# Kernel optimization log

Hardware: AMD Instinct MI355X
Metric: run time of the kernel (lower is better)

Reference implementation:

```python
import jax, jax.numpy as jnp
import numpy as np

NQ = 4
PI_HALF = np.pi / 2
HAD = jnp.array([[1, 1], [1, -1]], dtype=jnp.complex64) / np.sqrt(2)
CNOT = jnp.array([[1, 0, 0, 0], [0, 1, 0, 0], [0, 0, 0, 1], [0, 0, 1, 0]], dtype=jnp.complex64)
_bits = (np.arange(2 ** NQ)[:, None] >> np.arange(NQ - 1, -1, -1)[None, :]) & 1
ZSIGNS = jnp.asarray(1.0 - 2.0 * _bits, jnp.float32)  # [16, NQ]


def _ry(theta):
    c = jnp.cos(theta / 2).astype(jnp.complex64)
    s = jnp.sin(theta / 2).astype(jnp.complex64)
    return jnp.stack([jnp.stack([c, -s], -1), jnp.stack([s, c], -1)], -2)  # [...,2,2]


def _rot(phi, theta, omega):
    # PennyLane Rot = RZ(omega) @ RY(theta) @ RZ(phi)
    c = jnp.cos(theta / 2).astype(jnp.complex64)
    s = jnp.sin(theta / 2).astype(jnp.complex64)
    ep = jnp.exp(0.5j * phi).astype(jnp.complex64)
    eo = jnp.exp(0.5j * omega).astype(jnp.complex64)
    return jnp.stack([jnp.stack([jnp.conj(ep) * jnp.conj(eo) * c, -ep * jnp.conj(eo) * s]),
                      jnp.stack([jnp.conj(ep) * eo * s, ep * eo * c])])


def _cry(theta):
    # controlled-RY, batched: [B] -> [B,4,4], basis order (control, target)
    B = theta.shape[0]
    U = jnp.zeros((B, 4, 4), jnp.complex64).at[:, 0, 0].set(1.0).at[:, 1, 1].set(1.0)
    return U.at[:, 2:, 2:].set(_ry(theta))


def _apply1(state, U, wire):
    s = jnp.moveaxis(state, wire + 1, 1)
    shp = s.shape
    s = s.reshape(shp[0], 2, -1)
    s = jnp.einsum('ij,bjk->bik', U, s) if U.ndim == 2 else jnp.einsum('bij,bjk->bik', U, s)
    return jnp.moveaxis(s.reshape(shp), 1, wire + 1)


def _apply2(state, U, q0, q1):
    s = jnp.moveaxis(state, (q0 + 1, q1 + 1), (1, 2))
    shp = s.shape
    s = s.reshape(shp[0], 4, -1)
    s = jnp.einsum('ij,bjk->bik', U, s) if U.ndim == 2 else jnp.einsum('bij,bjk->bik', U, s)
    return jnp.moveaxis(s.reshape(shp), (1, 2), (q0 + 1, q1 + 1))


def _init_state(B):
    s = jnp.zeros((B, 2 ** NQ), jnp.complex64).at[:, 0].set(1.0)
    return s.reshape((B,) + (2,) * NQ)


def _zexp(state):
    p = state.reshape(state.shape[0], -1)
    p = p.real ** 2 + p.imag ** 2
    return p @ ZSIGNS  # [B, NQ]


def _attention_circuit(q, k, params):
    # q, k: [E, NQ] angles; params: [NQ, 3] shared
    s = _init_state(q.shape[0])
    for i in range(NQ):
        s = _apply1(s, _ry(q[:, i]), i)
    for i in range(NQ):
        s = _apply1(s, HAD, i)
    for i in range(NQ):
        s = _apply2(s, _cry(k[:, i]), i, (i + 1) % NQ)
    for i in range(NQ):
        s = _apply1(s, _rot(params[i, 0], params[i, 1], params[i, 2]), i)
    return _zexp(s)


def _entangle_circuit(x, params):
    # x: [N, NQ] angles; params: [n_layers, NQ, 3]
    s = _init_state(x.shape[0])
    for i in range(NQ):
        s = _apply1(s, _ry(x[:, i]), i)
    for l in range(params.shape[0]):
        for i in range(NQ - 1):
            s = _apply2(s, CNOT, i, i + 1)
        for i in range(NQ):
            s = _apply1(s, _rot(params[l, i, 0], params[l, i, 1], params[l, i, 2]), i)
        s = _apply2(s, CNOT, 0, NQ - 1)  # n_qubits >= 4
    return _zexp(s)


def _path_circuit(x, params):
    # x: [N, NQ]; params: [3, NQ, 3]
    s = _init_state(x.shape[0])
    for i in range(NQ):
        s = _apply1(s, HAD, i)
    for i in range(NQ):
        s = _apply1(s, _ry(x[:, i]), i)
    for l in range(3):
        for i in range(NQ):
            s = _apply1(s, _rot(params[l, i, 0], params[l, i, 1], params[l, i, 2]), i)
        for i in range(NQ - 1):
            s = _apply2(s, CNOT, i, i + 1)
    return _zexp(s)


def _forward(x, W_in, b_in, lin_W, lin_b, qproj_W, qproj_b, ent_params,
             attq_W, attq_b, attk_W, attk_b, att_qp, path_params,
             path_in_W, path_in_b, path_out_W, path_out_b, out_W, out_b, edge_index):
    N = x.shape[0]
    loops = jnp.arange(N, dtype=edge_index.dtype)
    ei = jnp.concatenate([edge_index, jnp.stack([loops, loops])], axis=1)  # add_self_loops
    src, dst = ei[0], ei[1]
    h = jax.nn.relu(x @ W_in.T + b_in)
    for l in range(lin_W.shape[0]):
        x_cls = h @ lin_W[l].T + lin_b[l]
        xq = _entangle_circuit(jnp.tanh(h[:, :NQ]) * PI_HALF, ent_params[l])
        x_comb = x_cls + xq @ qproj_W[l].T + qproj_b[l]
        q = jnp.tanh(h @ attq_W[l].T + attq_b[l]) * PI_HALF
        k = jnp.tanh(h @ attk_W[l].T + attk_b[l]) * PI_HALF
        scores = _attention_circuit(q[src], k[dst], att_qp[l]).mean(axis=1)  # [E]
        att = jax.nn.softmax(scores)  # global softmax over all edges (faithful)
        h = jax.ops.segment_sum(att[:, None] * x_comb[src], dst, num_segments=N)
        h = jax.nn.relu(h)  # dropout is identity at eval
    pq = jnp.tanh(h @ path_in_W.T + path_in_b) * PI_HALF
    h = _path_circuit(pq, path_params) @ path_out_W.T + path_out_b
    return h @ out_W.T + out_b


def setup_inputs() -> dict:
    key = jax.random.key(0)
    ks = jax.random.split(key, 22)
    N, E, D_in, D_h, D_out, L = 20000, 300000, 64, 128, 32, 2
    w = lambda k, shape: jax.random.normal(k, shape, jnp.float32) * 0.1
    return {
        'x': jax.random.normal(ks[0], (N, D_in), jnp.float32),
        'W_in': w(ks[1], (D_h, D_in)), 'b_in': w(ks[2], (D_h,)),
        'lin_W': w(ks[3], (L, D_h, D_h)), 'lin_b': w(ks[4], (L, D_h)),
        'qproj_W': w(ks[5], (L, D_h, NQ)), 'qproj_b': w(ks[6], (L, D_h)),
        'ent_params': w(ks[7], (L, 2, NQ, 3)),
        'attq_W': w(ks[8], (L, NQ, D_h)), 'attq_b': w(ks[9], (L, NQ)),
        'attk_W': w(ks[10], (L, NQ, D_h)), 'attk_b': w(ks[11], (L, NQ)),
        'att_qp': w(ks[12], (L, NQ, 3)),
        'path_params': w(ks[13], (3, NQ, 3)),
        'path_in_W': w(ks[14], (NQ, D_h)), 'path_in_b': w(ks[15], (NQ,)),
        'path_out_W': w(ks[16], (D_h, NQ)), 'path_out_b': w(ks[17], (D_h,)),
        'out_W': w(ks[18], (D_out, D_h)), 'out_b': w(ks[19], (D_out,)),
        'edge_index': jax.random.randint(ks[20], (2, E), 0, N, dtype=jnp.int32),
    }


def reference(x, W_in, b_in, lin_W, lin_b, qproj_W, qproj_b, ent_params,
              attq_W, attq_b, attk_W, attk_b, att_qp, path_params,
              path_in_W, path_in_b, path_out_W, path_out_b, out_W, out_b, edge_index):
    return _forward(x, W_in, b_in, lin_W, lin_b, qproj_W, qproj_b, ent_params,
                    attq_W, attq_b, attk_W, attk_b, att_qp, path_params,
                    path_in_W, path_in_b, path_out_W, path_out_b, out_W, out_b, edge_index)
```

## Files before the change

### kernel.cpp

```cpp
#include <hip/hip_runtime.h>
#include <math.h>

#define PI_HALF 1.57079632679489662f

__device__ __forceinline__ float fast_tanh(float x) {
    float e = __expf(2.f * x);
    return 1.f - 2.f * __builtin_amdgcn_rcpf(e + 1.f);
}


__device__ __forceinline__ void init_state(float sr[16], float si[16]) {
#pragma unroll
    for (int i = 0; i < 16; ++i) { sr[i] = 0.f; si[i] = 0.f; }
    sr[0] = 1.f;
}

template<int M>
__device__ __forceinline__ void ry_g(float sr[16], float si[16], float c, float s) {
#pragma unroll
    for (int i = 0; i < 16; ++i) {
        if (i & M) continue;
        const int j = i | M;
        float ar = sr[i], ai = si[i], br = sr[j], bi = si[j];
        sr[i] = c * ar - s * br;  si[i] = c * ai - s * bi;
        sr[j] = s * ar + c * br;  si[j] = s * ai + c * bi;
    }
}

template<int M>
__device__ __forceinline__ void had_g(float sr[16], float si[16]) {
    const float r = 0.70710678118654752f;
#pragma unroll
    for (int i = 0; i < 16; ++i) {
        if (i & M) continue;
        const int j = i | M;
        float ar = sr[i], ai = si[i], br = sr[j], bi = si[j];
        sr[i] = (ar + br) * r;  si[i] = (ai + bi) * r;
        sr[j] = (ar - br) * r;  si[j] = (ai - bi) * r;
    }
}

template<int MC, int MT>
__device__ __forceinline__ void cnot_g(float sr[16], float si[16]) {
#pragma unroll
    for (int i = 0; i < 16; ++i) {
        if (!(i & MC) || (i & MT)) continue;
        const int j = i | MT;
        float tr = sr[i], ti = si[i];
        sr[i] = sr[j]; si[i] = si[j];
        sr[j] = tr;    si[j] = ti;
    }
}

template<int MC, int MT>
__device__ __forceinline__ void cry_g(float sr[16], float si[16], float c, float s) {
#pragma unroll
    for (int i = 0; i < 16; ++i) {
        if (!(i & MC) || (i & MT)) continue;
        const int j = i | MT;
        float ar = sr[i], ai = si[i], br = sr[j], bi = si[j];
        sr[i] = c * ar - s * br;  si[i] = c * ai - s * bi;
        sr[j] = s * ar + c * br;  si[j] = s * ai + c * bi;
    }
}

template<int M>
__device__ __forceinline__ void rot_pre(float sr[16], float si[16], const float* __restrict__ u) {
    const float u00r = u[0], u00i = u[1], u01r = u[2], u01i = u[3];
    const float u10r = u[4], u10i = u[5], u11r = u[6], u11i = u[7];
#pragma unroll
    for (int i = 0; i < 16; ++i) {
        if (i & M) continue;
        const int j = i | M;
        float ar = sr[i], ai = si[i], br = sr[j], bi = si[j];
        sr[i] = u00r * ar - u00i * ai + u01r * br - u01i * bi;
        si[i] = u00r * ai + u00i * ar + u01r * bi + u01i * br;
        sr[j] = u10r * ar - u10i * ai + u11r * br - u11i * bi;
        si[j] = u10r * ai + u10i * ar + u11r * bi + u11i * br;
    }
}

__device__ __forceinline__ void zexp_g(const float sr[16], const float si[16], float z[4]) {
    float p[16];
#pragma unroll
    for (int i = 0; i < 16; ++i) p[i] = sr[i] * sr[i] + si[i] * si[i];
    z[0] = z[1] = z[2] = z[3] = 0.f;
#pragma unroll
    for (int i = 0; i < 16; ++i) {
        z[0] += (i & 8) ? -p[i] : p[i];
        z[1] += (i & 4) ? -p[i] : p[i];
        z[2] += (i & 2) ? -p[i] : p[i];
        z[3] += (i & 1) ? -p[i] : p[i];
    }
}

__global__ void k_setup(const float* __restrict__ entp, const float* __restrict__ attqp,
                        const float* __restrict__ pparm,
                        const float* __restrict__ outW, const float* __restrict__ outb,
                        const float* __restrict__ poW, const float* __restrict__ pob,
                        float* __restrict__ rotbuf, float* __restrict__ M,
                        float* __restrict__ v) {
    const int t = threadIdx.x;
    if (t < 36) {
        const float* p;
        if (t < 16)      p = entp  + t * 3;
        else if (t < 24) p = attqp + (t - 16) * 3;
        else             p = pparm + (t - 24) * 3;
        float phi = p[0], theta = p[1], omega = p[2];
        float st, ct; sincosf(0.5f * theta, &st, &ct);
        float sp, cp; sincosf(0.5f * (phi + omega), &sp, &cp);
        float sm, cm; sincosf(0.5f * (phi - omega), &sm, &cm);
        float* u = rotbuf + t * 8;
        u[0] =  ct * cp;  u[1] = -ct * sp;
        u[2] = -st * cm;  u[3] = -st * sm;
        u[4] =  st * cm;  u[5] = -st * sm;
        u[6] =  ct * cp;  u[7] =  ct * sp;
    } else if (t >= 64 && t < 192) {
        int t2 = t - 64;
        int o = t2 >> 2, i = t2 & 3;
        float acc = 0.f;
        for (int j = 0; j < 128; ++j) acc += outW[o * 128 + j] * poW[j * 4 + i];
        M[t2] = acc;
    } else if (t >= 192 && t < 224) {
        int o = t - 192;
        float acc = outb[o];
        for (int j = 0; j < 128; ++j) acc += outW[o * 128 + j] * pob[j];
        v[o] = acc;
    }
}


__global__ void k_hist(const int* __restrict__ ei, int* __restrict__ cnt, int E, int EP) {
    int e = blockIdx.x * blockDim.x + threadIdx.x;
    if (e >= EP) return;
    int d_ = (e < E) ? ei[E + e] : e - E;
    atomicAdd(&cnt[d_], 1);
}

__global__ void k_scan(const int* __restrict__ cnt, int* __restrict__ off,
                       int* __restrict__ cur, int N) {
    __shared__ int tot[1024];
    const int t = threadIdx.x;
    const int chunk = (N + 1023) >> 10;
    const int s0 = t * chunk;
    const int s1 = min(s0 + chunk, N);
    int sum = 0;
    for (int i = s0; i < s1; ++i) sum += cnt[i];
    tot[t] = sum;
    __syncthreads();
    for (int d = 1; d < 1024; d <<= 1) {
        int v = (t >= d) ? tot[t - d] : 0;
        __syncthreads();
        tot[t] += v;
        __syncthreads();
    }
    int run = (t == 0) ? 0 : tot[t - 1];
    for (int i = s0; i < s1; ++i) {
        off[i] = run; cur[i] = run;
        run += cnt[i];
    }
}

__global__ void k_fill(const int* __restrict__ ei, int* __restrict__ cur,
                       int* __restrict__ srcs, int* __restrict__ dsts, int E, int EP) {
    int e = blockIdx.x * blockDim.x + threadIdx.x;
    if (e >= EP) return;
    int s_, d_;
    if (e < E) { s_ = ei[e]; d_ = ei[E + e]; } else { s_ = d_ = e - E; }
    int pos = atomicAdd(&cur[d_], 1);
    srcs[pos] = s_;
    dsts[pos] = d_;
}


#define XS 68
__global__ __launch_bounds__(256) void k_in(
        const float* __restrict__ x, const float* __restrict__ W,
        const float* __restrict__ b, float* __restrict__ h, int N) {
    __shared__ float xs[16 * XS];
    const int base = blockIdx.x * 16;
    const int tid = threadIdx.x;
    for (int idx = tid; idx < 16 * 64; idx += 256) {
        int n = base + (idx >> 6);
        xs[(idx >> 6) * XS + (idx & 63)] = (n < N) ? x[(size_t)n * 64 + (idx & 63)] : 0.f;
    }
    __syncthreads();
    const int o  = tid & 127;
    const int nh = tid >> 7;
    float acc[8];
#pragma unroll
    for (int i = 0; i < 8; ++i) acc[i] = 0.f;
    const float4* w4 = (const float4*)(W + o * 64);
    for (int c4 = 0; c4 < 16; ++c4) {
        float4 w = w4[c4];
#pragma unroll
        for (int i = 0; i < 8; ++i) {
            float4 hv = *(const float4*)&xs[(nh * 8 + i) * XS + c4 * 4];
            acc[i] += w.x * hv.x + w.y * hv.y + w.z * hv.z + w.w * hv.w;
        }
    }
    const float bb = b[o];
#pragma unroll
    for (int i = 0; i < 8; ++i) {
        int node = base + nh * 8 + i;
        if (node < N) h[(size_t)node * 128 + o] = fmaxf(acc[i] + bb, 0.f);
    }
}

#define HS 132
__global__ __launch_bounds__(256) void k_lin(
        const float* __restrict__ h,
        const float* __restrict__ linW, const float* __restrict__ linb,
        const float* __restrict__ qpW, const float* __restrict__ qpb,
        const float* __restrict__ aqW, const float* __restrict__ aqb,
        const float* __restrict__ akW, const float* __restrict__ akb,
        const float* __restrict__ rotE,
        float* __restrict__ xcomb, float* __restrict__ qbuf,
        float* __restrict__ kbuf, int N) {
    __shared__ float hs[16 * HS];
    __shared__ float zS[16 * 4];
    const int base = blockIdx.x * 16;
    const int tid = threadIdx.x;
    for (int idx = tid; idx < 16 * 128; idx += 256) {
        int n = base + (idx >> 7);
        hs[(idx >> 7) * HS + (idx & 127)] = (n < N) ? h[(size_t)n * 128 + (idx & 127)] : 0.f;
    }
    __syncthreads();

    const int o  = tid & 127;
    const int nh = tid >> 7;
    float acc[8];
#pragma unroll
    for (int i = 0; i < 8; ++i) acc[i] = 0.f;
    const float4* w4 = (const float4*)(linW + o * 128);
    for (int c4 = 0; c4 < 32; ++c4) {
        float4 w = w4[c4];
#pragma unroll
        for (int i = 0; i < 8; ++i) {
            float4 hv = *(const float4*)&hs[(nh * 8 + i) * HS + c4 * 4];
            acc[i] += w.x * hv.x + w.y * hv.y + w.z * hv.z + w.w * hv.w;
        }
    }

    if (tid < 128) {
        const int nl = tid >> 3;
        const int which = tid & 7;
        const int qi = which & 3;
        const float4* Wp4 = (const float4*)(((which < 4) ? aqW : akW) + qi * 128);
        float dot = (which < 4) ? aqb[qi] : akb[qi];
        for (int c4 = 0; c4 < 32; ++c4) {
            float4 w = Wp4[c4];
            float4 hv = *(const float4*)&hs[nl * HS + c4 * 4];
            dot += w.x * hv.x + w.y * hv.y + w.z * hv.z + w.w * hv.w;
        }
        int node = base + nl;
        if (node < N) {
            float half = fast_tanh(dot) * (0.5f * PI_HALF);
            float s, c; __sincosf(half, &s, &c);
            float* dst = ((which < 4) ? qbuf : kbuf) + (size_t)node * 8 + qi * 2;
            dst[0] = c; dst[1] = s;
        }
    } else if (tid < 144) {
        const int en = tid - 128;
        float4 hv = *(const float4*)&hs[en * HS];
        float sr[16], si[16];
        init_state(sr, si);
        { float s, c; __sincosf(fast_tanh(hv.x) * (0.5f * PI_HALF), &s, &c); ry_g<8>(sr, si, c, s); }
        { float s, c; __sincosf(fast_tanh(hv.y) * (0.5f * PI_HALF), &s, &c); ry_g<4>(sr, si, c, s); }
        { float s, c; __sincosf(fast_tanh(hv.z) * (0.5f * PI_HALF), &s, &c); ry_g<2>(sr, si, c, s); }
        { float s, c; __sincosf(fast_tanh(hv.w) * (0.5f * PI_HALF), &s, &c); ry_g<1>(sr, si, c, s); }
#pragma unroll
        for (int l = 0; l < 2; ++l) {
            cnot_g<8, 4>(sr, si); cnot_g<4, 2>(sr, si); cnot_g<2, 1>(sr, si);
            const float* P = rotE + l * 32;
            rot_pre<8>(sr, si, P);
            rot_pre<4>(sr, si, P + 8);
            rot_pre<2>(sr, si, P + 16);
            rot_pre<1>(sr, si, P + 24);
            cnot_g<8, 1>(sr, si);
        }
        float z[4]; zexp_g(sr, si, z);
        zS[en * 4 + 0] = z[0]; zS[en * 4 + 1] = z[1];
        zS[en * 4 + 2] = z[2]; zS[en * 4 + 3] = z[3];
    }
    __syncthreads();

    const float bb = linb[o] + qpb[o];
    const float4 qw = *(const float4*)(qpW + o * 4);
#pragma unroll
    for (int i = 0; i < 8; ++i) {
        int node = base + nh * 8 + i;
        if (node < N) {
            float4 z = *(const float4*)&zS[(nh * 8 + i) * 4];
            xcomb[(size_t)node * 128 + o] = acc[i] + bb
                + qw.x * z.x + qw.y * z.y + qw.z * z.z + qw.w * z.w;
        }
    }
}

__global__ void k_att(const float* __restrict__ qb, const float* __restrict__ kb,
                      const int* __restrict__ srcs, const int* __restrict__ dsts,
                      const float* __restrict__ RA, float* __restrict__ escore,
                      float* __restrict__ sumexp, int EP) {
    __shared__ float red[4];
    int p = blockIdx.x * blockDim.x + threadIdx.x;
    float ex = 0.f;
    if (p < EP) {
        int s_ = srcs[p], d_ = dsts[p];
        float4 qa = *(const float4*)&qb[(size_t)s_ * 8];
        float4 qc = *(const float4*)&qb[(size_t)s_ * 8 + 4];
        float4 ka = *(const float4*)&kb[(size_t)d_ * 8];
        float4 kc = *(const float4*)&kb[(size_t)d_ * 8 + 4];
        float sr[16], si[16];
        init_state(sr, si);
        ry_g<8>(sr, si, qa.x, qa.y);
        ry_g<4>(sr, si, qa.z, qa.w);
        ry_g<2>(sr, si, qc.x, qc.y);
        ry_g<1>(sr, si, qc.z, qc.w);
        had_g<8>(sr, si); had_g<4>(sr, si); had_g<2>(sr, si); had_g<1>(sr, si);
        cry_g<8, 4>(sr, si, ka.x, ka.y);
        cry_g<4, 2>(sr, si, ka.z, ka.w);
        cry_g<2, 1>(sr, si, kc.x, kc.y);
        cry_g<1, 8>(sr, si, kc.z, kc.w);
        rot_pre<8>(sr, si, RA);
        rot_pre<4>(sr, si, RA + 8);
        rot_pre<2>(sr, si, RA + 16);
        rot_pre<1>(sr, si, RA + 24);
        float z[4]; zexp_g(sr, si, z);
        float sc = 0.25f * (z[0] + z[1] + z[2] + z[3]);
        ex = __expf(sc);
        escore[p] = ex;
    }
    float w = ex;
#pragma unroll
    for (int d = 32; d > 0; d >>= 1) w += __shfl_down(w, d, 64);
    if ((threadIdx.x & 63) == 0) red[threadIdx.x >> 6] = w;
    __syncthreads();
    if (threadIdx.x == 0)
        atomicAdd(sumexp, red[0] + red[1] + red[2] + red[3]);
}

__global__ void k_gather(const float* __restrict__ xcomb, const int* __restrict__ srcs,
                         const float* __restrict__ escore, const int* __restrict__ off,
                         const int* __restrict__ cnt, const float* __restrict__ sumexp,
                         float* __restrict__ h) {
    __shared__ int sS[128];
    __shared__ float wS[128];
    const int b = blockIdx.x;
    const int tid = threadIdx.x;
    const int start = off[b];
    const int num = cnt[b];
    float acc = 0.f;
    for (int base = 0; base < num; base += 128) {
        int m = min(128, num - base);
        if (tid < m) {
            sS[tid] = srcs[start + base + tid];
            wS[tid] = escore[start + base + tid];
        }
        __syncthreads();
        for (int i = 0; i < m; ++i)
            acc += wS[i] * xcomb[(size_t)sS[i] * 128 + tid];
        __syncthreads();
    }
    const float invS = __builtin_amdgcn_rcpf(sumexp[0]);
    h[(size_t)b * 128 + tid] = fmaxf(acc * invS, 0.f);
}

__global__ __launch_bounds__(256) void k_path(
        const float* __restrict__ h, const float* __restrict__ piW,
        const float* __restrict__ pib, const float* __restrict__ RP,
        const float* __restrict__ M, const float* __restrict__ v,
        float* __restrict__ out, int N) {
    __shared__ float hs[64 * HS];
    __shared__ float pqS[64 * 9];
    __shared__ float zS[64 * 4];
    __shared__ float MS[128];
    __shared__ float vS[32];
    const int base = blockIdx.x * 64;
    const int tid = threadIdx.x;
    if (tid < 128) MS[tid] = M[tid];
    else if (tid < 160) vS[tid - 128] = v[tid - 128];
    for (int idx = tid; idx < 64 * 128; idx += 256) {
        int n = base + (idx >> 7);
        hs[(idx >> 7) * HS + (idx & 127)] = (n < N) ? h[(size_t)n * 128 + (idx & 127)] : 0.f;
    }
    __syncthreads();
    {
        const int nl = tid >> 2;
        const int i  = tid & 3;
        float dot = pib[i];
        const float4* w4 = (const float4*)(piW + i * 128);
        for (int c4 = 0; c4 < 32; ++c4) {
            float4 w = w4[c4];
            float4 hv = *(const float4*)&hs[nl * HS + c4 * 4];
            dot += w.x * hv.x + w.y * hv.y + w.z * hv.z + w.w * hv.w;
        }
        float half = fast_tanh(dot) * (0.5f * PI_HALF);
        float s, c; __sincosf(half, &s, &c);
        pqS[nl * 9 + i * 2]     = c;
        pqS[nl * 9 + i * 2 + 1] = s;
    }
    __syncthreads();
    if (tid < 64) {
        const float* p = pqS + tid * 9;
        float sr[16], si[16];
        init_state(sr, si);
        had_g<8>(sr, si); had_g<4>(sr, si); had_g<2>(sr, si); had_g<1>(sr, si);
        ry_g<8>(sr, si, p[0], p[1]);
        ry_g<4>(sr, si, p[2], p[3]);
        ry_g<2>(sr, si, p[4], p[5]);
        ry_g<1>(sr, si, p[6], p[7]);
#pragma unroll
        for (int l = 0; l < 3; ++l) {
            const float* P = RP + l * 32;
            rot_pre<8>(sr, si, P);
            rot_pre<4>(sr, si, P + 8);
            rot_pre<2>(sr, si, P + 16);
            rot_pre<1>(sr, si, P + 24);
            cnot_g<8, 4>(sr, si); cnot_g<4, 2>(sr, si); cnot_g<2, 1>(sr, si);
        }
        float z[4]; zexp_g(sr, si, z);
        zS[tid * 4 + 0] = z[0]; zS[tid * 4 + 1] = z[1];
        zS[tid * 4 + 2] = z[2]; zS[tid * 4 + 3] = z[3];
    }
    __syncthreads();
#pragma unroll
    for (int k = 0; k < 8; ++k) {
        int flat = k * 256 + tid;
        int nl = flat >> 5;
        int o = flat & 31;
        int node = base + nl;
        if (node < N) {
            out[(size_t)node * 32 + o] = vS[o]
                + MS[o * 4 + 0] * zS[nl * 4 + 0] + MS[o * 4 + 1] * zS[nl * 4 + 1]
                + MS[o * 4 + 2] * zS[nl * 4 + 2] + MS[o * 4 + 3] * zS[nl * 4 + 3];
        }
    }
}


extern "C" void kernel_launch(void* const* d_in, const int* in_sizes, int n_in,
                              void* d_out, int out_size, void* d_ws, size_t ws_size,
                              hipStream_t stream) {
    const float* x     = (const float*)d_in[0];
    const float* W_in  = (const float*)d_in[1];
    const float* b_in  = (const float*)d_in[2];
    const float* linW  = (const float*)d_in[3];
    const float* linb  = (const float*)d_in[4];
    const float* qpW   = (const float*)d_in[5];
    const float* qpb   = (const float*)d_in[6];
    const float* entp  = (const float*)d_in[7];
    const float* aqW   = (const float*)d_in[8];
    const float* aqb   = (const float*)d_in[9];
    const float* akW   = (const float*)d_in[10];
    const float* akb   = (const float*)d_in[11];
    const float* attqp = (const float*)d_in[12];
    const float* pparm = (const float*)d_in[13];
    const float* piW   = (const float*)d_in[14];
    const float* pib   = (const float*)d_in[15];
    const float* poW   = (const float*)d_in[16];
    const float* pob   = (const float*)d_in[17];
    const float* outW  = (const float*)d_in[18];
    const float* outb  = (const float*)d_in[19];
    const int*   ei    = (const int*)d_in[20];

    const int N  = in_sizes[0] / 64;
    const int E  = in_sizes[20] / 2;
    const int EP = E + N;

    float* ws     = (float*)d_ws;
    float* h      = ws;
    float* xcomb  = h      + (size_t)N * 128;
    float* qbuf   = xcomb  + (size_t)N * 128;
    float* kbuf   = qbuf   + (size_t)N * 8;
    float* escore = kbuf   + (size_t)N * 8;
    float* rotbuf = escore + EP;
    float* Mm     = rotbuf + 36 * 8;
    float* vv     = Mm + 128;
    int*   cnt    = (int*)(vv + 32);
    float* sumexp = (float*)(cnt + N);
    int*   off    = (int*)(sumexp + 4);
    int*   cur    = off + N;
    int*   srcs   = cur + N;
    int*   dsts   = srcs + EP;

    const float* rotE = rotbuf;
    const float* rotA = rotbuf + 128;
    const float* rotP = rotbuf + 192;

    const int nb16 = (N + 15) / 16;
    const int ebl  = (EP + 255) / 256;

    hipMemsetAsync(cnt, 0, (size_t)(N + 4) * sizeof(int), stream);
    k_hist<<<ebl, 256, 0, stream>>>(ei, cnt, E, EP);
    k_scan<<<1, 1024, 0, stream>>>(cnt, off, cur, N);
    k_fill<<<ebl, 256, 0, stream>>>(ei, cur, srcs, dsts, E, EP);
    k_setup<<<1, 256, 0, stream>>>(entp, attqp, pparm, outW, outb, poW, pob,
                                   rotbuf, Mm, vv);
    k_in<<<nb16, 256, 0, stream>>>(x, W_in, b_in, h, N);

    for (int l = 0; l < 2; ++l) {
        k_lin<<<nb16, 256, 0, stream>>>(h,
            linW + (size_t)l * 128 * 128, linb + l * 128,
            qpW + (size_t)l * 128 * 4, qpb + l * 128,
            aqW + (size_t)l * 4 * 128, aqb + l * 4,
            akW + (size_t)l * 4 * 128, akb + l * 4,
            rotE + l * 64, xcomb, qbuf, kbuf, N);
        k_att<<<ebl, 256, 0, stream>>>(qbuf, kbuf, srcs, dsts, rotA + l * 32,
                                       escore, sumexp + l, EP);
        k_gather<<<N, 128, 0, stream>>>(xcomb, srcs, escore, off, cnt, sumexp + l, h);
    }

    k_path<<<(N + 63) / 64, 256, 0, stream>>>(h, piW, pib, rotP, Mm, vv,
                                              (float*)d_out, N);
}
```

Before: 415.5 us.

## Register-tile node-linear GEMMs and split entanglement circuit into separate kernel

Reworks the input and per-layer linear kernels so each thread computes a 4x4 block of outputs by nodes, with 32 nodes per block, increasing weight and shared-memory reuse and vectorising stores. The entanglement quantum circuit, previously run by 16 threads of the linear block while others waited, moves to its own per-node kernel that writes z-expectations to a workspace buffer read by the linear kernel. This removes the serial circuit from the GEMM's critical path and barrier, at the cost of an extra launch per layer and fewer blocks for the GEMMs.

```diff
diff --git a/kernel.cpp b/kernel.cpp
--- a/kernel.cpp
+++ b/kernel.cpp
@@ -177,72 +177,136 @@
 __global__ __launch_bounds__(256) void k_in(
         const float* __restrict__ x, const float* __restrict__ W,
         const float* __restrict__ b, float* __restrict__ h, int N) {
-    __shared__ float xs[16 * XS];
-    const int base = blockIdx.x * 16;
+    __shared__ float xs[32 * XS];
+    const int base = blockIdx.x * 32;
     const int tid = threadIdx.x;
-    for (int idx = tid; idx < 16 * 64; idx += 256) {
+    for (int idx = tid; idx < 32 * 64; idx += 256) {
         int n = base + (idx >> 6);
         xs[(idx >> 6) * XS + (idx & 63)] = (n < N) ? x[(size_t)n * 64 + (idx & 63)] : 0.f;
     }
     __syncthreads();
-    const int o  = tid & 127;
-    const int nh = tid >> 7;
-    float acc[8];
-#pragma unroll
-    for (int i = 0; i < 8; ++i) acc[i] = 0.f;
-    const float4* w4 = (const float4*)(W + o * 64);
+    const int og = tid & 31;
+    const int ng = tid >> 5;
+    float acc[4][4];
+#pragma unroll
+    for (int r = 0; r < 4; ++r)
+#pragma unroll
+        for (int n = 0; n < 4; ++n) acc[r][n] = 0.f;
     for (int c4 = 0; c4 < 16; ++c4) {
-        float4 w = w4[c4];
-#pragma unroll
-        for (int i = 0; i < 8; ++i) {
-            float4 hv = *(const float4*)&xs[(nh * 8 + i) * XS + c4 * 4];
-            acc[i] += w.x * hv.x + w.y * hv.y + w.z * hv.z + w.w * hv.w;
-        }
-    }
-    const float bb = b[o];
-#pragma unroll
-    for (int i = 0; i < 8; ++i) {
-        int node = base + nh * 8 + i;
-        if (node < N) h[(size_t)node * 128 + o] = fmaxf(acc[i] + bb, 0.f);
-    }
+        float4 wv[4], hv[4];
+#pragma unroll
+        for (int r = 0; r < 4; ++r) wv[r] = *(const float4*)&W[(og * 4 + r) * 64 + c4 * 4];
+#pragma unroll
+        for (int n = 0; n < 4; ++n) hv[n] = *(const float4*)&xs[(ng * 4 + n) * XS + c4 * 4];
+#pragma unroll
+        for (int r = 0; r < 4; ++r)
+#pragma unroll
+            for (int n = 0; n < 4; ++n)
+                acc[r][n] += wv[r].x * hv[n].x + wv[r].y * hv[n].y
+                           + wv[r].z * hv[n].z + wv[r].w * hv[n].w;
+    }
+    const float4 bb = *(const float4*)&b[og * 4];
+#pragma unroll
+    for (int n = 0; n < 4; ++n) {
+        int node = base + ng * 4 + n;
+        if (node < N) {
+            float4 o4 = make_float4(fmaxf(acc[0][n] + bb.x, 0.f),
+                                    fmaxf(acc[1][n] + bb.y, 0.f),
+                                    fmaxf(acc[2][n] + bb.z, 0.f),
+                                    fmaxf(acc[3][n] + bb.w, 0.f));
+            *(float4*)&h[(size_t)node * 128 + og * 4] = o4;
+        }
+    }
+}
+
+__global__ void k_ent(const float* __restrict__ h, const float* __restrict__ rotE,
+                      float* __restrict__ xq, int N) {
+    int n = blockIdx.x * blockDim.x + threadIdx.x;
+    if (n >= N) return;
+    float4 hv = *(const float4*)&h[(size_t)n * 128];
+    float sr[16], si[16];
+    init_state(sr, si);
+    { float s, c; __sincosf(fast_tanh(hv.x) * (0.5f * PI_HALF), &s, &c); ry_g<8>(sr, si, c, s); }
+    { float s, c; __sincosf(fast_tanh(hv.y) * (0.5f * PI_HALF), &s, &c); ry_g<4>(sr, si, c, s); }
+    { float s, c; __sincosf(fast_tanh(hv.z) * (0.5f * PI_HALF), &s, &c); ry_g<2>(sr, si, c, s); }
+    { float s, c; __sincosf(fast_tanh(hv.w) * (0.5f * PI_HALF), &s, &c); ry_g<1>(sr, si, c, s); }
+#pragma unroll
+    for (int l = 0; l < 2; ++l) {
+        cnot_g<8, 4>(sr, si); cnot_g<4, 2>(sr, si); cnot_g<2, 1>(sr, si);
+        const float* P = rotE + l * 32;
+        rot_pre<8>(sr, si, P);
+        rot_pre<4>(sr, si, P + 8);
+        rot_pre<2>(sr, si, P + 16);
+        rot_pre<1>(sr, si, P + 24);
+        cnot_g<8, 1>(sr, si);
+    }
+    float z[4]; zexp_g(sr, si, z);
+    *(float4*)&xq[(size_t)n * 4] = make_float4(z[0], z[1], z[2], z[3]);
 }
 
 #define HS 132
 __global__ __launch_bounds__(256) void k_lin(
-        const float* __restrict__ h,
+        const float* __restrict__ h, const float* __restrict__ xq,
         const float* __restrict__ linW, const float* __restrict__ linb,
         const float* __restrict__ qpW, const float* __restrict__ qpb,
         const float* __restrict__ aqW, const float* __restrict__ aqb,
         const float* __restrict__ akW, const float* __restrict__ akb,
-        const float* __restrict__ rotE,
         float* __restrict__ xcomb, float* __restrict__ qbuf,
         float* __restrict__ kbuf, int N) {
-    __shared__ float hs[16 * HS];
-    __shared__ float zS[16 * 4];
-    const int base = blockIdx.x * 16;
+    __shared__ float hs[32 * HS];
+    __shared__ float zS[32 * 4];
+    const int base = blockIdx.x * 32;
     const int tid = threadIdx.x;
-    for (int idx = tid; idx < 16 * 128; idx += 256) {
+    for (int idx = tid; idx < 32 * 128; idx += 256) {
         int n = base + (idx >> 7);
         hs[(idx >> 7) * HS + (idx & 127)] = (n < N) ? h[(size_t)n * 128 + (idx & 127)] : 0.f;
     }
-    __syncthreads();
-
-    const int o  = tid & 127;
-    const int nh = tid >> 7;
-    float acc[8];
-#pragma unroll
-    for (int i = 0; i < 8; ++i) acc[i] = 0.f;
-    const float4* w4 = (const float4*)(linW + o * 128);
+    if (tid < 128) {
+        int n = base + (tid >> 2);
+        zS[tid] = (n < N) ? xq[(size_t)n * 4 + (tid & 3)] : 0.f;
+    }
+    __syncthreads();
+
+    const int og = tid & 31;
+    const int ng = tid >> 5;
+    float acc[4][4];
+#pragma unroll
+    for (int r = 0; r < 4; ++r)
+#pragma unroll
+        for (int n = 0; n < 4; ++n) acc[r][n] = 0.f;
     for (int c4 = 0; c4 < 32; ++c4) {
-        float4 w = w4[c4];
-#pragma unroll
-        for (int i = 0; i < 8; ++i) {
-            float4 hv = *(const float4*)&hs[(nh * 8 + i) * HS + c4 * 4];
-            acc[i] += w.x * hv.x + w.y * hv.y + w.z * hv.z + w.w * hv.w;
-        }
-    }
-
-    if (tid < 128) {
+        float4 wv[4], hv[4];
+#pragma unroll
+        for (int r = 0; r < 4; ++r) wv[r] = *(const float4*)&linW[(og * 4 + r) * 128 + c4 * 4];
+#pragma unroll
+        for (int n = 0; n < 4; ++n) hv[n] = *(const float4*)&hs[(ng * 4 + n) * HS + c4 * 4];
+#pragma unroll
+        for (int r = 0; r < 4; ++r)
+#pragma unroll
+            for (int n = 0; n < 4; ++n)
+                acc[r][n] += wv[r].x * hv[n].x + wv[r].y * hv[n].y
+                           + wv[r].z * hv[n].z + wv[r].w * hv[n].w;
+    }
+    const float4 lb = *(const float4*)&linb[og * 4];
+    const float4 qb4 = *(const float4*)&qpb[og * 4];
+    float4 qw[4];
+#pragma unroll
+    for (int r = 0; r < 4; ++r) qw[r] = *(const float4*)&qpW[(og * 4 + r) * 4];
+#pragma unroll
+    for (int n = 0; n < 4; ++n) {
+        int node = base + ng * 4 + n;
+        if (node < N) {
+            float4 z = *(const float4*)&zS[(ng * 4 + n) * 4];
+            float4 o4;
+            o4.x = acc[0][n] + lb.x + qb4.x + qw[0].x * z.x + qw[0].y * z.y + qw[0].z * z.z + qw[0].w * z.w;
+            o4.y = acc[1][n] + lb.y + qb4.y + qw[1].x * z.x + qw[1].y * z.y + qw[1].z * z.z + qw[1].w * z.w;
+            o4.z = acc[2][n] + lb.z + qb4.z + qw[2].x * z.x + qw[2].y * z.y + qw[2].z * z.z + qw[2].w * z.w;
+            o4.w = acc[3][n] + lb.w + qb4.w + qw[3].x * z.x + qw[3].y * z.y + qw[3].z * z.z + qw[3].w * z.w;
+            *(float4*)&xcomb[(size_t)node * 128 + og * 4] = o4;
+        }
+    }
+
+    {
         const int nl = tid >> 3;
         const int which = tid & 7;
         const int qi = which & 3;
@@ -259,41 +323,6 @@
             float s, c; __sincosf(half, &s, &c);
             float* dst = ((which < 4) ? qbuf : kbuf) + (size_t)node * 8 + qi * 2;
             dst[0] = c; dst[1] = s;
-        }
-    } else if (tid < 144) {
-        const int en = tid - 128;
-        float4 hv = *(const float4*)&hs[en * HS];
-        float sr[16], si[16];
-        init_state(sr, si);
-        { float s, c; __sincosf(fast_tanh(hv.x) * (0.5f * PI_HALF), &s, &c); ry_g<8>(sr, si, c, s); }
-        { float s, c; __sincosf(fast_tanh(hv.y) * (0.5f * PI_HALF), &s, &c); ry_g<4>(sr, si, c, s); }
-        { float s, c; __sincosf(fast_tanh(hv.z) * (0.5f * PI_HALF), &s, &c); ry_g<2>(sr, si, c, s); }
-        { float s, c; __sincosf(fast_tanh(hv.w) * (0.5f * PI_HALF), &s, &c); ry_g<1>(sr, si, c, s); }
-#pragma unroll
-        for (int l = 0; l < 2; ++l) {
-            cnot_g<8, 4>(sr, si); cnot_g<4, 2>(sr, si); cnot_g<2, 1>(sr, si);
-            const float* P = rotE + l * 32;
-            rot_pre<8>(sr, si, P);
-            rot_pre<4>(sr, si, P + 8);
-            rot_pre<2>(sr, si, P + 16);
-            rot_pre<1>(sr, si, P + 24);
-            cnot_g<8, 1>(sr, si);
-        }
-        float z[4]; zexp_g(sr, si, z);
-        zS[en * 4 + 0] = z[0]; zS[en * 4 + 1] = z[1];
-        zS[en * 4 + 2] = z[2]; zS[en * 4 + 3] = z[3];
-    }
-    __syncthreads();
-
-    const float bb = linb[o] + qpb[o];
-    const float4 qw = *(const float4*)(qpW + o * 4);
-#pragma unroll
-    for (int i = 0; i < 8; ++i) {
-        int node = base + nh * 8 + i;
-        if (node < N) {
-            float4 z = *(const float4*)&zS[(nh * 8 + i) * 4];
-            xcomb[(size_t)node * 128 + o] = acc[i] + bb
-                + qw.x * z.x + qw.y * z.y + qw.z * z.z + qw.w * z.w;
         }
     }
 }
@@ -471,7 +500,8 @@
     float* ws     = (float*)d_ws;
     float* h      = ws;
     float* xcomb  = h      + (size_t)N * 128;
-    float* qbuf   = xcomb  + (size_t)N * 128;
+    float* xq     = xcomb  + (size_t)N * 128;
+    float* qbuf   = xq     + (size_t)N * 4;
     float* kbuf   = qbuf   + (size_t)N * 8;
     float* escore = kbuf   + (size_t)N * 8;
     float* rotbuf = escore + EP;
@@ -488,7 +518,7 @@
     const float* rotA = rotbuf + 128;
     const float* rotP = rotbuf + 192;
 
-    const int nb16 = (N + 15) / 16;
+    const int nb32 = (N + 31) / 32;
     const int ebl  = (EP + 255) / 256;
 
     hipMemsetAsync(cnt, 0, (size_t)(N + 4) * sizeof(int), stream);
@@ -497,15 +527,16 @@
     k_fill<<<ebl, 256, 0, stream>>>(ei, cur, srcs, dsts, E, EP);
     k_setup<<<1, 256, 0, stream>>>(entp, attqp, pparm, outW, outb, poW, pob,
                                    rotbuf, Mm, vv);
-    k_in<<<nb16, 256, 0, stream>>>(x, W_in, b_in, h, N);
+    k_in<<<nb32, 256, 0, stream>>>(x, W_in, b_in, h, N);
 
     for (int l = 0; l < 2; ++l) {
-        k_lin<<<nb16, 256, 0, stream>>>(h,
+        k_ent<<<(N + 255) / 256, 256, 0, stream>>>(h, rotE + l * 64, xq, N);
+        k_lin<<<nb32, 256, 0, stream>>>(h, xq,
             linW + (size_t)l * 128 * 128, linb + l * 128,
             qpW + (size_t)l * 128 * 4, qpb + l * 128,
             aqW + (size_t)l * 4 * 128, aqb + l * 4,
             akW + (size_t)l * 4 * 128, akb + l * 4,
-            rotE + l * 64, xcomb, qbuf, kbuf, N);
+            xcomb, qbuf, kbuf, N);
         k_att<<<ebl, 256, 0, stream>>>(qbuf, kbuf, srcs, dsts, rotA + l * 32,
                                        escore, sumexp + l, EP);
         k_gather<<<N, 128, 0, stream>>>(xcomb, srcs, escore, off, cnt, sumexp + l, h);
```

New measurement: 454.5 us. 1.09x slower.
